# Optimization experiments

Measured on AMD Instinct MI355X. Metric: run time of the kernel, lower is better.

The kernel has to match this reference:

```python
import jax, jax.numpy as jnp
import numpy as np

B, S, D, H = 2, 2048, 1024, 16
HD = D // H  # head_dim = 64


def setup_inputs() -> dict:
    key = jax.random.key(0)
    ks = jax.random.split(key, 12)
    scale = 1.0 / np.sqrt(D)
    inp = {
        "query": jax.random.normal(ks[0], (B, S, D), dtype=jnp.float32),
        "key_in": jax.random.normal(ks[1], (B, S, D), dtype=jnp.float32),
        "value": jax.random.normal(ks[2], (B, S, D), dtype=jnp.float32),
        "mask": jnp.zeros((B, S), dtype=bool),
        # nn.Linear weights stored as [out, in] like torch; y = x @ W.T + b
        "Wq": jax.random.normal(ks[3], (D, D), dtype=jnp.float32) * scale,
        "bq": jnp.zeros((D,), dtype=jnp.float32),
        "Wk": jax.random.normal(ks[4], (D, D), dtype=jnp.float32) * scale,
        "bk": jnp.zeros((D,), dtype=jnp.float32),
        "Wv": jax.random.normal(ks[5], (D, D), dtype=jnp.float32) * scale,
        "bv": jnp.zeros((D,), dtype=jnp.float32),
        "Wo": jax.random.normal(ks[6], (D, D), dtype=jnp.float32) * scale,
        "bo": jnp.zeros((D,), dtype=jnp.float32),
    }
    return inp


def reference(query, key_in, value, mask, Wq, bq, Wk, bk, Wv, bv, Wo, bo):
    def split_heads(x):  # [B,S,D] -> [B,H,S,HD]
        return x.reshape(B, -1, H, HD).transpose(0, 2, 1, 3)

    Q = split_heads(query @ Wq.T + bq)
    K = split_heads(key_in @ Wk.T + bk)
    V = split_heads(value @ Wv.T + bv)

    scores = jnp.einsum("bhqd,bhkd->bhqk", Q, K) / np.sqrt(HD)
    # key-padding mask: True -> -inf, broadcast over heads and query positions
    scores = jnp.where(mask[:, None, None, :], -jnp.inf, scores)
    attn = jax.nn.softmax(scores, axis=-1)
    out = jnp.einsum("bhqk,bhkd->bhqd", attn, V)  # [B,H,S,HD]
    out = out.transpose(0, 2, 1, 3).reshape(B, -1, D)
    return out @ Wo.T + bo
```

## Files before the change

kernel.cpp:

```cpp
#include <hip/hip_runtime.h>

typedef __attribute__((ext_vector_type(8))) __bf16 bf16x8;
typedef __attribute__((ext_vector_type(4))) float f32x4;
typedef __attribute__((ext_vector_type(16))) float f32x16;
typedef __attribute__((ext_vector_type(4))) unsigned int u32x4;
typedef unsigned short us;

#define SEQ 2048
#define DIM 1024
#define NH 16
#define HDIM 64

#define QSCALE 0.1803368801111204f

__device__ inline us f2bf(float f) {
    unsigned u = __builtin_bit_cast(unsigned, f);
    u += 0x7FFFu + ((u >> 16) & 1u);
    return (us)(u >> 16);
}

__device__ inline unsigned sx32(unsigned v) {
    return (unsigned)__shfl_xor((int)v, 32);
}

__global__ __launch_bounds__(256) void cast_many(
    const float* __restrict__ s0, const float* __restrict__ s1,
    const float* __restrict__ s2, const float* __restrict__ s3,
    us* __restrict__ dst, int n_each)
{
    const float* src = (blockIdx.y == 0) ? s0 : (blockIdx.y == 1) ? s1
                     : (blockIdx.y == 2) ? s2 : s3;
    size_t base = (size_t)blockIdx.y * (size_t)n_each;
    int i = (blockIdx.x * 256 + threadIdx.x) * 4;
    if (i < n_each) {
        float4 v = *(const float4*)(src + i);
        ushort4 o;
        o.x = f2bf(v.x); o.y = f2bf(v.y); o.z = f2bf(v.z); o.w = f2bf(v.w);
        *(ushort4*)(dst + base + i) = o;
    }
}

__global__ __launch_bounds__(64) void maskpack(
    const unsigned char* __restrict__ mask, unsigned* __restrict__ mw)
{
    int t = blockIdx.x * 64 + threadIdx.x;
    unsigned wv = 0;
#pragma unroll
    for (int j = 0; j < 32; j++) wv |= (mask[t * 32 + j] ? 1u : 0u) << j;
    mw[t] = wv;
}

#define BM 128
#define BN 128
#define BK 64

__device__ __forceinline__ void gemm_core(
    const us* __restrict__ A, const us* __restrict__ W,
    const float* __restrict__ bias, void* __restrict__ out,
    int M, int N, int K, int mode, float oscale)
{
    __shared__ us lA[BM * BK];
    __shared__ us lB[BN * BK];

    const int tid  = threadIdx.x;
    const int lane = tid & 63;
    const int w    = tid >> 6;
    const int wm   = w >> 1, wn = w & 1;
    const int m0   = blockIdx.y * BM, n0 = blockIdx.x * BN;
    const int g    = lane >> 4, li = lane & 15;

    const f32x4 fz = {0.f, 0.f, 0.f, 0.f};
    f32x4 acc[4][4];
#pragma unroll
    for (int i = 0; i < 4; i++)
#pragma unroll
        for (int j = 0; j < 4; j++) acc[i][j] = fz;

    for (int k0 = 0; k0 < K; k0 += BK) {
#pragma unroll
        for (int i = 0; i < 4; i++) {
            int v = tid + i * 256;
            int row = v >> 3, c8 = (v & 7) * 8;
            *(uint4*)&lA[row * BK + c8] =
                *(const uint4*)&A[(size_t)(m0 + row) * K + k0 + c8];
            *(uint4*)&lB[row * BK + c8] =
                *(const uint4*)&W[(size_t)(n0 + row) * K + k0 + c8];
        }
        __syncthreads();
#pragma unroll
        for (int kk = 0; kk < 2; kk++) {
            bf16x8 af[4], bfr[4];
#pragma unroll
            for (int i = 0; i < 4; i++)
                af[i] = *(const bf16x8*)&lA[(wm * 64 + i * 16 + li) * BK + kk * 32 + g * 8];
#pragma unroll
            for (int j = 0; j < 4; j++)
                bfr[j] = *(const bf16x8*)&lB[(wn * 64 + j * 16 + li) * BK + kk * 32 + g * 8];
#pragma unroll
            for (int i = 0; i < 4; i++)
#pragma unroll
                for (int j = 0; j < 4; j++)
                    acc[i][j] = __builtin_amdgcn_mfma_f32_16x16x32_bf16(
                        af[i], bfr[j], acc[i][j], 0, 0, 0);
        }
        __syncthreads();
    }

    const int r0 = g * 4;
#pragma unroll
    for (int i = 0; i < 4; i++) {
#pragma unroll
        for (int j = 0; j < 4; j++) {
            int col = n0 + wn * 64 + j * 16 + li;
            float bs = bias[col];
#pragma unroll
            for (int r = 0; r < 4; r++) {
                int row = m0 + wm * 64 + i * 16 + r0 + r;
                float val = (acc[i][j][r] + bs) * oscale;
                if (mode == 2) {
                    ((float*)out)[(size_t)row * N + col] = val;
                } else {
                    int b = row >> 11, s = row & (SEQ - 1);
                    int h = col >> 6, hd = col & (HDIM - 1);
                    size_t idx = (mode == 0)
                        ? ((((size_t)b * NH + h) * SEQ + s) * HDIM + hd)
                        : ((((size_t)b * NH + h) * HDIM + hd) * SEQ + s);
                    ((us*)out)[idx] = f2bf(val);
                }
            }
        }
    }
}

__global__ __launch_bounds__(256) void gemm_qkv(
    const us* __restrict__ xq, const us* __restrict__ xk, const us* __restrict__ xv,
    const us* __restrict__ wq, const us* __restrict__ wk, const us* __restrict__ wv,
    const float* __restrict__ bq, const float* __restrict__ bk, const float* __restrict__ bv,
    us* __restrict__ Qb, us* __restrict__ Kb, us* __restrict__ VTb)
{
    int z = blockIdx.z;
    if (z == 0)      gemm_core(xq, wq, bq, Qb,  2 * SEQ, DIM, DIM, 0, QSCALE);
    else if (z == 1) gemm_core(xk, wk, bk, Kb,  2 * SEQ, DIM, DIM, 0, 1.0f);
    else             gemm_core(xv, wv, bv, VTb, 2 * SEQ, DIM, DIM, 1, 1.0f);
}

__global__ __launch_bounds__(256) void gemm_one(
    const us* __restrict__ A, const us* __restrict__ W,
    const float* __restrict__ bias, float* __restrict__ out)
{
    gemm_core(A, W, bias, out, 2 * SEQ, DIM, DIM, 2, 1.0f);
}

__global__ __launch_bounds__(256) void attn_fwd2(
    const us* __restrict__ Qb, const us* __restrict__ Kb,
    const us* __restrict__ VT, const unsigned* __restrict__ mw,
    us* __restrict__ out)
{
    const int tid  = threadIdx.x;
    const int w    = tid >> 6, lane = tid & 63;
    const int tile = blockIdx.x * 4 + w;
    const int bh   = tile >> 6, qt = tile & 63;
    const int b    = bh >> 4, h = bh & 15;
    const int q0   = qt * 32;
    const int ql   = lane & 31, hi = lane >> 5;

    const us* Qp  = Qb + (((size_t)bh * SEQ) + q0 + ql) * HDIM + hi * 8;
    const us* Kp  = Kb + ((size_t)bh * SEQ + ql) * HDIM + hi * 8;
    const us* Vp0 = VT + ((size_t)bh * HDIM + ql) * SEQ + hi * 8;
    const us* Vp1 = Vp0 + 32 * SEQ;

    bf16x8 qf[4];
#pragma unroll
    for (int t = 0; t < 4; t++) qf[t] = *(const bf16x8*)(Qp + t * 16);

    f32x16 o0 = {0,0,0,0,0,0,0,0,0,0,0,0,0,0,0,0};
    f32x16 o1 = {0,0,0,0,0,0,0,0,0,0,0,0,0,0,0,0};
    const f32x16 z16 = {0,0,0,0,0,0,0,0,0,0,0,0,0,0,0,0};
    float mrun = -1e30f, lrun = 0.f;

    bf16x8 kf[4];
#pragma unroll
    for (int t = 0; t < 4; t++) kf[t] = *(const bf16x8*)(Kp + t * 16);

    for (int kv = 0; kv < SEQ; kv += 32) {
        bf16x8 vf0[2], vf1[2];
#pragma unroll
        for (int t = 0; t < 2; t++) {
            vf0[t] = *(const bf16x8*)(Vp0 + kv + t * 16);
            vf1[t] = *(const bf16x8*)(Vp1 + kv + t * 16);
        }

        f32x16 s = z16;
#pragma unroll
        for (int t = 0; t < 4; t++)
            s = __builtin_amdgcn_mfma_f32_32x32x16_bf16(kf[t], qf[t], s, 0, 0, 0);

        if (kv + 32 < SEQ) {
            const us* Kn = Kp + (size_t)(kv + 32) * HDIM;
#pragma unroll
            for (int t = 0; t < 4; t++) kf[t] = *(const bf16x8*)(Kn + t * 16);
        }

        unsigned m32 = (unsigned)__builtin_amdgcn_readfirstlane(
            (int)mw[b * 64 + (kv >> 5)]);

        float pmax = s[0];
#pragma unroll
        for (int r = 1; r < 16; r++) pmax = fmaxf(pmax, s[r]);
        pmax = fmaxf(pmax, __shfl_xor(pmax, 32));

        float nm   = fmaxf(mrun, pmax);
        float corr = __builtin_amdgcn_exp2f(mrun - nm);
        float p[16];
#pragma unroll
        for (int r = 0; r < 16; r++) p[r] = __builtin_amdgcn_exp2f(s[r] - nm);
        if (m32) {
            unsigned ms = hi ? (m32 >> 4) : m32;
#pragma unroll
            for (int r = 0; r < 16; r++)
                if ((ms >> ((r & 3) + 8 * (r >> 2))) & 1) p[r] = 0.f;
        }
        float ps = 0.f;
#pragma unroll
        for (int r = 0; r < 16; r++) ps += p[r];
        ps += __shfl_xor(ps, 32);

        lrun = lrun * corr + ps;
        mrun = nm;
#pragma unroll
        for (int j = 0; j < 16; j++) { o0[j] *= corr; o1[j] *= corr; }

        unsigned pw[8];
#pragma unroll
        for (int j = 0; j < 8; j++)
            asm("v_cvt_pk_bf16_f32 %0, %1, %2"
                : "=v"(pw[j]) : "v"(p[2 * j]), "v"(p[2 * j + 1]));

        unsigned x0 = sx32(pw[0]), x1 = sx32(pw[1]), x2 = sx32(pw[2]), x3 = sx32(pw[3]);
        unsigned x4 = sx32(pw[4]), x5 = sx32(pw[5]), x6 = sx32(pw[6]), x7 = sx32(pw[7]);

        u32x4 t0, t1;
        t0.x = hi ? x2    : pw[0];
        t0.y = hi ? x3    : pw[1];
        t0.z = hi ? pw[2] : x0;
        t0.w = hi ? pw[3] : x1;
        t1.x = hi ? x6    : pw[4];
        t1.y = hi ? x7    : pw[5];
        t1.z = hi ? pw[6] : x4;
        t1.w = hi ? pw[7] : x5;
        bf16x8 pa0 = __builtin_bit_cast(bf16x8, t0);
        bf16x8 pa1 = __builtin_bit_cast(bf16x8, t1);

        o0 = __builtin_amdgcn_mfma_f32_32x32x16_bf16(vf0[0], pa0, o0, 0, 0, 0);
        o0 = __builtin_amdgcn_mfma_f32_32x32x16_bf16(vf0[1], pa1, o0, 0, 0, 0);
        o1 = __builtin_amdgcn_mfma_f32_32x32x16_bf16(vf1[0], pa0, o1, 0, 0, 0);
        o1 = __builtin_amdgcn_mfma_f32_32x32x16_bf16(vf1[1], pa1, o1, 0, 0, 0);
    }

    float inv = __builtin_amdgcn_rcpf(lrun);
    us* op = out + ((size_t)b * SEQ + q0 + ql) * DIM + h * HDIM + 4 * hi;
#pragma unroll
    for (int g2 = 0; g2 < 4; g2++) {
        ushort4 v0, v1;
        v0.x = f2bf(o0[4 * g2 + 0] * inv); v0.y = f2bf(o0[4 * g2 + 1] * inv);
        v0.z = f2bf(o0[4 * g2 + 2] * inv); v0.w = f2bf(o0[4 * g2 + 3] * inv);
        v1.x = f2bf(o1[4 * g2 + 0] * inv); v1.y = f2bf(o1[4 * g2 + 1] * inv);
        v1.z = f2bf(o1[4 * g2 + 2] * inv); v1.w = f2bf(o1[4 * g2 + 3] * inv);
        *(ushort4*)(op + 8 * g2)      = v0;
        *(ushort4*)(op + 32 + 8 * g2) = v1;
    }
}

extern "C" void kernel_launch(void* const* d_in, const int* in_sizes, int n_in,
                              void* d_out, int out_size, void* d_ws, size_t ws_size,
                              hipStream_t stream)
{
    const float* q  = (const float*)d_in[0];
    const float* k  = (const float*)d_in[1];
    const float* v  = (const float*)d_in[2];
    const unsigned char* mask = (const unsigned char*)d_in[3];
    const float* Wq = (const float*)d_in[4];
    const float* bq = (const float*)d_in[5];
    const float* Wk = (const float*)d_in[6];
    const float* bk = (const float*)d_in[7];
    const float* Wv = (const float*)d_in[8];
    const float* bv = (const float*)d_in[9];
    const float* Wo = (const float*)d_in[10];
    const float* bo = (const float*)d_in[11];

    us* ws  = (us*)d_ws;
    us* xq  = ws;
    us* xk  = ws + 4194304;
    us* xv  = ws + 8388608;
    us* wqb = ws + 12582912;
    us* wkb = ws + 13631488;
    us* wvb = ws + 14680064;
    us* wob = ws + 15728640;
    us* Qb  = ws + 16777216;
    us* Kb  = ws + 20971520;
    us* VTb = ws + 25165824;
    us* AO  = ws + 29360128;
    unsigned* mwords = (unsigned*)(ws + 33554432);

    cast_many<<<dim3(4096, 3), 256, 0, stream>>>(q, k, v, q, xq, 4194304);
    cast_many<<<dim3(1024, 4), 256, 0, stream>>>(Wq, Wk, Wv, Wo, wqb, 1048576);
    maskpack<<<dim3(2), 64, 0, stream>>>(mask, mwords);

    gemm_qkv<<<dim3(DIM / BN, (2 * SEQ) / BM, 3), 256, 0, stream>>>(
        xq, xk, xv, wqb, wkb, wvb, bq, bk, bv, Qb, Kb, VTb);

    attn_fwd2<<<dim3(512), 256, 0, stream>>>(Qb, Kb, VTb, mwords, AO);

    gemm_one<<<dim3(DIM / BN, (2 * SEQ) / BM), 256, 0, stream>>>(AO, wob, bo, (float*)d_out);
}
```

Before: 320.1 us.

## Split attention KV range in two with combine pass, lazy rescale, LDS direct loads

Splits the attention KV sequence into two halves processed by separate waves, which doubles the grid. Each half writes fp16 partial outputs plus max and sum, and a new combine kernel merges them. The online softmax now skips rescaling unless the max grows by more than a threshold, and the per-iteration cross-lane reductions are deferred or reduced. The GEMM tile loads now use global_load_lds direct-to-LDS transfers. This adds a partial-result write and re-read, an extra launch, and fp16 intermediate precision.

```diff
diff --git a/kernel.cpp b/kernel.cpp
--- a/kernel.cpp
+++ b/kernel.cpp
@@ -4,6 +4,8 @@
 typedef __attribute__((ext_vector_type(4))) float f32x4;
 typedef __attribute__((ext_vector_type(16))) float f32x16;
 typedef __attribute__((ext_vector_type(4))) unsigned int u32x4;
+typedef __attribute__((ext_vector_type(8))) _Float16 f16x8;
+typedef __attribute__((ext_vector_type(4))) _Float16 f16x4;
 typedef unsigned short us;
 
 #define SEQ 2048
@@ -21,6 +23,12 @@
 
 __device__ inline unsigned sx32(unsigned v) {
     return (unsigned)__shfl_xor((int)v, 32);
+}
+
+__device__ __forceinline__ void gload16(const us* g, us* l) {
+    __builtin_amdgcn_global_load_lds(
+        (const __attribute__((address_space(1))) unsigned int*)(const void*)g,
+        (__attribute__((address_space(3))) unsigned int*)(void*)l, 16, 0, 0);
 }
 
 __global__ __launch_bounds__(256) void cast_many(
@@ -81,10 +89,8 @@
         for (int i = 0; i < 4; i++) {
             int v = tid + i * 256;
             int row = v >> 3, c8 = (v & 7) * 8;
-            *(uint4*)&lA[row * BK + c8] =
-                *(const uint4*)&A[(size_t)(m0 + row) * K + k0 + c8];
-            *(uint4*)&lB[row * BK + c8] =
-                *(const uint4*)&W[(size_t)(n0 + row) * K + k0 + c8];
+            gload16(&A[(size_t)(m0 + row) * K + k0 + c8], &lA[v * 8]);
+            gload16(&W[(size_t)(n0 + row) * K + k0 + c8], &lB[v * 8]);
         }
         __syncthreads();
 #pragma unroll
@@ -151,18 +157,20 @@
     gemm_core(A, W, bias, out, 2 * SEQ, DIM, DIM, 2, 1.0f);
 }
 
-__global__ __launch_bounds__(256) void attn_fwd2(
+__global__ __launch_bounds__(256, 4) void attn_split(
     const us* __restrict__ Qb, const us* __restrict__ Kb,
     const us* __restrict__ VT, const unsigned* __restrict__ mw,
-    us* __restrict__ out)
+    _Float16* __restrict__ opart, float* __restrict__ mlpart)
 {
     const int tid  = threadIdx.x;
     const int w    = tid >> 6, lane = tid & 63;
-    const int tile = blockIdx.x * 4 + w;
+    const int unit = blockIdx.x * 4 + w;
+    const int tile = unit >> 1, half = unit & 1;
     const int bh   = tile >> 6, qt = tile & 63;
-    const int b    = bh >> 4, h = bh & 15;
+    const int b    = bh >> 4;
     const int q0   = qt * 32;
     const int ql   = lane & 31, hi = lane >> 5;
+    const int kv0  = half * 1024, kv1 = kv0 + 1024;
 
     const us* Qp  = Qb + (((size_t)bh * SEQ) + q0 + ql) * HDIM + hi * 8;
     const us* Kp  = Kb + ((size_t)bh * SEQ + ql) * HDIM + hi * 8;
@@ -173,16 +181,25 @@
 #pragma unroll
     for (int t = 0; t < 4; t++) qf[t] = *(const bf16x8*)(Qp + t * 16);
 
-    f32x16 o0 = {0,0,0,0,0,0,0,0,0,0,0,0,0,0,0,0};
-    f32x16 o1 = {0,0,0,0,0,0,0,0,0,0,0,0,0,0,0,0};
     const f32x16 z16 = {0,0,0,0,0,0,0,0,0,0,0,0,0,0,0,0};
+    f32x16 o0 = z16, o1 = z16;
     float mrun = -1e30f, lrun = 0.f;
 
     bf16x8 kf[4];
 #pragma unroll
-    for (int t = 0; t < 4; t++) kf[t] = *(const bf16x8*)(Kp + t * 16);
-
-    for (int kv = 0; kv < SEQ; kv += 32) {
+    for (int t = 0; t < 4; t++) kf[t] = *(const bf16x8*)(Kp + (size_t)kv0 * HDIM + t * 16);
+
+    for (int kv = kv0; kv < kv1; kv += 32) {
+        f32x16 s = z16;
+#pragma unroll
+        for (int t = 0; t < 4; t++)
+            s = __builtin_amdgcn_mfma_f32_32x32x16_bf16(kf[t], qf[t], s, 0, 0, 0);
+
+        if (kv + 32 < kv1) {
+            const us* Kn = Kp + (size_t)(kv + 32) * HDIM;
+#pragma unroll
+            for (int t = 0; t < 4; t++) kf[t] = *(const bf16x8*)(Kn + t * 16);
+        }
         bf16x8 vf0[2], vf1[2];
 #pragma unroll
         for (int t = 0; t < 2; t++) {
@@ -190,45 +207,41 @@
             vf1[t] = *(const bf16x8*)(Vp1 + kv + t * 16);
         }
 
-        f32x16 s = z16;
-#pragma unroll
-        for (int t = 0; t < 4; t++)
-            s = __builtin_amdgcn_mfma_f32_32x32x16_bf16(kf[t], qf[t], s, 0, 0, 0);
-
-        if (kv + 32 < SEQ) {
-            const us* Kn = Kp + (size_t)(kv + 32) * HDIM;
-#pragma unroll
-            for (int t = 0; t < 4; t++) kf[t] = *(const bf16x8*)(Kn + t * 16);
-        }
-
         unsigned m32 = (unsigned)__builtin_amdgcn_readfirstlane(
             (int)mw[b * 64 + (kv >> 5)]);
 
-        float pmax = s[0];
-#pragma unroll
-        for (int r = 1; r < 16; r++) pmax = fmaxf(pmax, s[r]);
-        pmax = fmaxf(pmax, __shfl_xor(pmax, 32));
-
-        float nm   = fmaxf(mrun, pmax);
-        float corr = __builtin_amdgcn_exp2f(mrun - nm);
+        float t8[8];
+#pragma unroll
+        for (int j = 0; j < 8; j++) t8[j] = fmaxf(s[j], s[j + 8]);
+#pragma unroll
+        for (int j = 0; j < 4; j++) t8[j] = fmaxf(t8[j], t8[j + 4]);
+        float pmax = fmaxf(fmaxf(t8[0], t8[1]), fmaxf(t8[2], t8[3]));
+
+        if (!__all(pmax <= mrun + 8.f)) {
+            float pm = fmaxf(pmax, __shfl_xor(pmax, 32));
+            float nm = fmaxf(mrun, pm);
+            float corr = __builtin_amdgcn_exp2f(mrun - nm);
+            lrun *= corr;
+#pragma unroll
+            for (int j = 0; j < 16; j++) { o0[j] *= corr; o1[j] *= corr; }
+            mrun = nm;
+        }
+
         float p[16];
 #pragma unroll
-        for (int r = 0; r < 16; r++) p[r] = __builtin_amdgcn_exp2f(s[r] - nm);
+        for (int r = 0; r < 16; r++) p[r] = __builtin_amdgcn_exp2f(s[r] - mrun);
         if (m32) {
             unsigned ms = hi ? (m32 >> 4) : m32;
 #pragma unroll
             for (int r = 0; r < 16; r++)
                 if ((ms >> ((r & 3) + 8 * (r >> 2))) & 1) p[r] = 0.f;
         }
-        float ps = 0.f;
-#pragma unroll
-        for (int r = 0; r < 16; r++) ps += p[r];
-        ps += __shfl_xor(ps, 32);
-
-        lrun = lrun * corr + ps;
-        mrun = nm;
-#pragma unroll
-        for (int j = 0; j < 16; j++) { o0[j] *= corr; o1[j] *= corr; }
+        float a8[8];
+#pragma unroll
+        for (int j = 0; j < 8; j++) a8[j] = p[j] + p[j + 8];
+#pragma unroll
+        for (int j = 0; j < 4; j++) a8[j] += a8[j + 4];
+        lrun += (a8[0] + a8[1]) + (a8[2] + a8[3]);
 
         unsigned pw[8];
 #pragma unroll
@@ -236,18 +249,20 @@
             asm("v_cvt_pk_bf16_f32 %0, %1, %2"
                 : "=v"(pw[j]) : "v"(p[2 * j]), "v"(p[2 * j + 1]));
 
-        unsigned x0 = sx32(pw[0]), x1 = sx32(pw[1]), x2 = sx32(pw[2]), x3 = sx32(pw[3]);
-        unsigned x4 = sx32(pw[4]), x5 = sx32(pw[5]), x6 = sx32(pw[6]), x7 = sx32(pw[7]);
+        unsigned y0 = sx32(hi ? pw[0] : pw[2]);
+        unsigned y1 = sx32(hi ? pw[1] : pw[3]);
+        unsigned y2 = sx32(hi ? pw[4] : pw[6]);
+        unsigned y3 = sx32(hi ? pw[5] : pw[7]);
 
         u32x4 t0, t1;
-        t0.x = hi ? x2    : pw[0];
-        t0.y = hi ? x3    : pw[1];
-        t0.z = hi ? pw[2] : x0;
-        t0.w = hi ? pw[3] : x1;
-        t1.x = hi ? x6    : pw[4];
-        t1.y = hi ? x7    : pw[5];
-        t1.z = hi ? pw[6] : x4;
-        t1.w = hi ? pw[7] : x5;
+        t0.x = hi ? y0    : pw[0];
+        t0.y = hi ? y1    : pw[1];
+        t0.z = hi ? pw[2] : y0;
+        t0.w = hi ? pw[3] : y1;
+        t1.x = hi ? y2    : pw[4];
+        t1.y = hi ? y3    : pw[5];
+        t1.z = hi ? pw[6] : y2;
+        t1.w = hi ? pw[7] : y3;
         bf16x8 pa0 = __builtin_bit_cast(bf16x8, t0);
         bf16x8 pa1 = __builtin_bit_cast(bf16x8, t1);
 
@@ -257,18 +272,61 @@
         o1 = __builtin_amdgcn_mfma_f32_32x32x16_bf16(vf1[1], pa1, o1, 0, 0, 0);
     }
 
-    float inv = __builtin_amdgcn_rcpf(lrun);
-    us* op = out + ((size_t)b * SEQ + q0 + ql) * DIM + h * HDIM + 4 * hi;
+    float lh  = lrun + __shfl_xor(lrun, 32);
+    float inv = __builtin_amdgcn_rcpf(lh);
+
+    size_t orow = (size_t)half * 65536 + (size_t)bh * SEQ + q0 + ql;
+    _Float16* od = opart + orow * 64;
 #pragma unroll
     for (int g2 = 0; g2 < 4; g2++) {
-        ushort4 v0, v1;
-        v0.x = f2bf(o0[4 * g2 + 0] * inv); v0.y = f2bf(o0[4 * g2 + 1] * inv);
-        v0.z = f2bf(o0[4 * g2 + 2] * inv); v0.w = f2bf(o0[4 * g2 + 3] * inv);
-        v1.x = f2bf(o1[4 * g2 + 0] * inv); v1.y = f2bf(o1[4 * g2 + 1] * inv);
-        v1.z = f2bf(o1[4 * g2 + 2] * inv); v1.w = f2bf(o1[4 * g2 + 3] * inv);
-        *(ushort4*)(op + 8 * g2)      = v0;
-        *(ushort4*)(op + 32 + 8 * g2) = v1;
-    }
+        f16x4 v0, v1;
+#pragma unroll
+        for (int j = 0; j < 4; j++) {
+            v0[j] = (_Float16)(o0[4 * g2 + j] * inv);
+            v1[j] = (_Float16)(o1[4 * g2 + j] * inv);
+        }
+        *(f16x4*)(od + 8 * g2 + 4 * hi)      = v0;
+        *(f16x4*)(od + 32 + 8 * g2 + 4 * hi) = v1;
+    }
+    if (hi == 0) {
+        float2 mlv; mlv.x = mrun; mlv.y = lh;
+        *(float2*)&mlpart[orow * 2] = mlv;
+    }
+}
+
+__global__ __launch_bounds__(256) void attn_combine(
+    const _Float16* __restrict__ op, const float* __restrict__ ml,
+    us* __restrict__ AO)
+{
+    int t   = blockIdx.x * 256 + threadIdx.x;
+    int row = t >> 3, dc = (t & 7) * 8;
+    int bh  = row >> 11, q = row & (SEQ - 1);
+    int b   = bh >> 4, h = bh & 15;
+
+    float2 ml0 = *(const float2*)&ml[(size_t)row * 2];
+    float2 ml1 = *(const float2*)&ml[(size_t)(65536 + row) * 2];
+    float M  = fmaxf(ml0.x, ml1.x);
+    float w0 = ml0.y * __builtin_amdgcn_exp2f(ml0.x - M);
+    float w1 = ml1.y * __builtin_amdgcn_exp2f(ml1.x - M);
+    float wi = __builtin_amdgcn_rcpf(w0 + w1);
+    float a0 = w0 * wi, a1 = w1 * wi;
+
+    f16x8 v0 = *(const f16x8*)(op + (size_t)row * 64 + dc);
+    f16x8 v1 = *(const f16x8*)(op + 4194304 + (size_t)row * 64 + dc);
+
+    ushort4 r0, r1;
+    r0.x = f2bf(a0 * (float)v0[0] + a1 * (float)v1[0]);
+    r0.y = f2bf(a0 * (float)v0[1] + a1 * (float)v1[1]);
+    r0.z = f2bf(a0 * (float)v0[2] + a1 * (float)v1[2]);
+    r0.w = f2bf(a0 * (float)v0[3] + a1 * (float)v1[3]);
+    r1.x = f2bf(a0 * (float)v0[4] + a1 * (float)v1[4]);
+    r1.y = f2bf(a0 * (float)v0[5] + a1 * (float)v1[5]);
+    r1.z = f2bf(a0 * (float)v0[6] + a1 * (float)v1[6]);
+    r1.w = f2bf(a0 * (float)v0[7] + a1 * (float)v1[7]);
+
+    us* dst = AO + ((size_t)b * SEQ + q) * DIM + h * HDIM + dc;
+    *(ushort4*)dst       = r0;
+    *(ushort4*)(dst + 4) = r1;
 }
 
 extern "C" void kernel_launch(void* const* d_in, const int* in_sizes, int n_in,
@@ -301,6 +359,8 @@
     us* VTb = ws + 25165824;
     us* AO  = ws + 29360128;
     unsigned* mwords = (unsigned*)(ws + 33554432);
+    _Float16* opart  = (_Float16*)ws;
+    float*    mlpart = (float*)(ws + 8388608 + 524288);
 
     cast_many<<<dim3(4096, 3), 256, 0, stream>>>(q, k, v, q, xq, 4194304);
     cast_many<<<dim3(1024, 4), 256, 0, stream>>>(Wq, Wk, Wv, Wo, wqb, 1048576);
@@ -309,7 +369,8 @@
     gemm_qkv<<<dim3(DIM / BN, (2 * SEQ) / BM, 3), 256, 0, stream>>>(
         xq, xk, xv, wqb, wkb, wvb, bq, bk, bv, Qb, Kb, VTb);
 
-    attn_fwd2<<<dim3(512), 256, 0, stream>>>(Qb, Kb, VTb, mwords, AO);
+    attn_split<<<dim3(1024), 256, 0, stream>>>(Qb, Kb, VTb, mwords, opart, mlpart);
+    attn_combine<<<dim3(2048), 256, 0, stream>>>(opart, mlpart, AO);
 
     gemm_one<<<dim3(DIM / BN, (2 * SEQ) / BM), 256, 0, stream>>>(AO, wob, bo, (float*)d_out);
 }
```

Measured after the change: 328.8 us. +2.7%, slower.
